# Performance work log

Measured on AMD Instinct MI355X. Metric: run time of the kernel, lower is better.

Reference implementation:

```python
import jax, jax.numpy as jnp
import numpy as np

B, C, N = 4, 128, 8192
CQK = C // 4  # query/key projection dim = out_channels // 4


def setup_inputs() -> dict:
    key = jax.random.key(0)
    ks = jax.random.split(key, 9)
    s_in = 1.0 / np.sqrt(C)
    return {
        "x": jax.random.normal(ks[0], (B, C, N), dtype=jnp.float32),
        "xyz": jax.random.normal(ks[1], (B, N, 3), dtype=jnp.float32),
        "Wq": jax.random.normal(ks[2], (CQK, C), dtype=jnp.float32) * s_in,
        "bq": jax.random.normal(ks[3], (CQK,), dtype=jnp.float32) * 0.01,
        "Wk": jax.random.normal(ks[4], (CQK, C), dtype=jnp.float32) * s_in,
        "bk": jax.random.normal(ks[5], (CQK,), dtype=jnp.float32) * 0.01,
        "Wv": jax.random.normal(ks[6], (C, C), dtype=jnp.float32) * s_in,
        "bv": jax.random.normal(ks[7], (C,), dtype=jnp.float32) * 0.01,
        "gamma": jax.random.normal(ks[8], (1,), dtype=jnp.float32) * 0.1,
    }


def reference(x, xyz, Wq, bq, Wk, bk, Wv, bv, gamma):
    # 1x1 Conv1d == per-point linear projection over channels
    q = jnp.einsum('oc,bcn->bon', Wq, x) + bq[None, :, None]   # (B, CQK, N)
    k = jnp.einsum('oc,bcn->bon', Wk, x) + bk[None, :, None]   # (B, CQK, N)
    v = jnp.einsum('oc,bcn->bon', Wv, x) + bv[None, :, None]   # (B, C, N)

    # energy[b, n, m] = <q[:, n], k[:, m]>
    energy = jnp.einsum('bcn,bcm->bnm', q, k)                  # (B, N, N)

    # positional correlation bias: normalize coords per point, cosine-sim matrix
    xyz_bcn = jnp.swapaxes(xyz, 1, 2)                          # (B, 3, N)
    xyz_norm = xyz_bcn / (jnp.linalg.norm(xyz_bcn, axis=1, keepdims=True) + 1e-8)
    pos_corr = jnp.einsum('bcn,bcm->bnm', xyz_norm, xyz_norm)  # (B, N, N)
    energy = energy + 0.1 * pos_corr

    attention = jax.nn.softmax(energy, axis=-1)                # rowwise over m

    # out[b, c, n] = sum_m v[b, c, m] * attention[b, n, m]
    out = jnp.einsum('bcm,bnm->bcn', v, attention)             # (B, C, N)
    return gamma * out + x
```

## Files before the change

### kernel.cpp

```cpp
#include <hip/hip_runtime.h>

#define NPTS 8192
#define NB 4
#define NCH 128
#define DQK 48
#define TK 64
#define SPLIT 4
#define KEYS_PER (NPTS / SPLIT)
#define ROUNDS (KEYS_PER / TK)
#define SH2 28.853901f
#define LOG2E 1.4426950408889634f

typedef unsigned short ushort_t;
typedef unsigned int uint_t;
typedef __attribute__((ext_vector_type(8))) short bf16x8;
typedef __attribute__((ext_vector_type(4))) float f32x4;
typedef __attribute__((ext_vector_type(16))) float f32x16;

static __device__ __forceinline__ ushort_t f2bf(float x) {
  union { float f; uint_t u; } v; v.f = x;
  uint_t r = v.u + 0x7fffu + ((v.u >> 16) & 1u);
  return (ushort_t)(r >> 16);
}
static __device__ __forceinline__ float bf2f(ushort_t u) {
  union { uint_t i; float f; } v; v.i = ((uint_t)u) << 16; return v.f;
}
static __device__ __forceinline__ int sig16(int n) {
  int g2 = (n >> 2) & 3;
  return (g2 == 1 || g2 == 2) ? (n ^ 0xC) : n;
}

typedef __attribute__((address_space(1))) void void_g;
typedef __attribute__((address_space(3))) void void_l;
static __device__ __forceinline__ void gload_lds16(const ushort_t* g, ushort_t* l) {
  __builtin_amdgcn_global_load_lds((void_g*)(ushort_t*)g, (void_l*)l, 16, 0, 0);
}

__global__ __launch_bounds__(512, 1)
void wprep_kernel(const float* __restrict__ Wq, const float* __restrict__ bq,
                  const float* __restrict__ Wk, const float* __restrict__ bk,
                  const float* __restrict__ Wv, const float* __restrict__ bv,
                  ushort_t* __restrict__ Wb, float* __restrict__ bias_pre) {
  const int z = blockIdx.x;
  const int ks = threadIdx.x >> 6;
  const int lane = threadIdx.x & 63;
  const int l31 = lane & 31, h = lane >> 5;
  const float* W = (z == 0) ? Wq : (z == 1) ? Wk : (Wv + (size_t)(z - 2) * 32 * 128);
  const float sc = (z == 0) ? LOG2E : 1.0f;
  const float* wr = W + l31 * 128 + ks * 16 + h * 8;
  union { ushort_t u[8]; bf16x8 v; } p;
#pragma unroll
  for (int j = 0; j < 8; ++j) p.u[j] = f2bf(wr[j] * sc);
  *(bf16x8*)(Wb + ((size_t)(z * 8 + ks) * 64 + lane) * 8) = p.v;
  if (z == 0 && threadIdx.x < 192) {
    int i = threadIdx.x;
    bias_pre[i] = (i < 32) ? bq[i] * LOG2E : (i < 64) ? bk[i - 32] : bv[i - 64];
  }
}

__global__ __launch_bounds__(256, 4)
void projm2_kernel(const float* __restrict__ x, const float* __restrict__ xyz,
                   const ushort_t* __restrict__ Wb,
                   const float* __restrict__ bias_pre,
                   ushort_t* __restrict__ Qb, ushort_t* __restrict__ Kb,
                   ushort_t* __restrict__ Vt) {
  const int tid = threadIdx.x;
  const int lane = tid & 63, wv = tid >> 6;
  const int l31 = lane & 31, h = lane >> 5;
  const int b = blockIdx.y;
  const int n = blockIdx.x * 128 + wv * 32 + l31;

  bf16x8 bfr[8];
  const float* xb = x + (size_t)b * NCH * NPTS + n;
#pragma unroll
  for (int ks = 0; ks < 8; ++ks) {
    const float* xc = xb + (size_t)(ks * 16 + h * 8) * NPTS;
    union { ushort_t u[8]; bf16x8 v; } p;
#pragma unroll
    for (int j = 0; j < 8; ++j) p.u[j] = f2bf(xc[(size_t)j * NPTS]);
    bfr[ks] = p.v;
  }

  float xa = xyz[((size_t)b * NPTS + n) * 3 + 0];
  float xc2 = xyz[((size_t)b * NPTS + n) * 3 + 1];
  float xd = xyz[((size_t)b * NPTS + n) * 3 + 2];
  float rinv = 1.0f / (sqrtf(xa * xa + xc2 * xc2 + xd * xd) + 1e-8f);

#pragma unroll 1
  for (int z = 0; z < 6; ++z) {
    f32x16 S;
#pragma unroll
    for (int r = 0; r < 16; ++r)
      S[r] = bias_pre[z * 32 + (r & 3) + 8 * (r >> 2) + 4 * h];
#pragma unroll
    for (int ks = 0; ks < 8; ++ks) {
      bf16x8 af = *(const bf16x8*)(Wb + ((size_t)(z * 8 + ks) * 64 + lane) * 8);
      S = __builtin_amdgcn_mfma_f32_32x32x16_bf16(af, bfr[ks], S, 0, 0, 0);
    }
    if (z <= 1) {
      float sc = (z == 0) ? LOG2E : 1.0f;
      ushort_t* dst = (z == 0 ? Qb : Kb) + ((size_t)b * NPTS + n) * DQK;
#pragma unroll
      for (int r = 0; r < 16; ++r)
        dst[(r & 3) + 8 * (r >> 2) + 4 * h] = f2bf(S[r]);
      float rn = 0.31622776601683794f * sc * rinv;
      union { ushort_t u[16]; bf16x8 v[2]; } t;
#pragma unroll
      for (int j = 0; j < 16; ++j) t.u[j] = 0;
      t.u[0] = f2bf(xa * rn); t.u[1] = f2bf(xc2 * rn); t.u[2] = f2bf(xd * rn);
      *(bf16x8*)(dst + 32) = t.v[0];
      *(bf16x8*)(dst + 40) = t.v[1];
    } else {
      const int np = (n & ~15) | sig16(n & 15);
      const int c0 = (z - 2) * 32;
#pragma unroll
      for (int r = 0; r < 16; ++r)
        Vt[((size_t)b * NCH + c0 + (r & 3) + 8 * (r >> 2) + 4 * h) * NPTS + np] =
            f2bf(S[r]);
    }
  }
}

__global__ __launch_bounds__(512, 2)
void attn32_kernel(const ushort_t* __restrict__ Qb, const ushort_t* __restrict__ Kb,
                   const ushort_t* __restrict__ Vt,
                   ushort_t* __restrict__ PACC, float* __restrict__ PL) {
  __shared__ __align__(16) ushort_t L[2][22][512];
  const int tid = threadIdx.x;
  const int lane = tid & 63, w = tid >> 6;
  const int l31 = lane & 31, h = lane >> 5;

  const int lin = blockIdx.x;
  const int bs = lin & 15;
  const int b = bs & 3, sseg = bs >> 2;
  const int qblk = lin >> 4;
  const int q0w = qblk * 512 + w * 64;
  const int m00 = sseg * KEYS_PER;

  bf16x8 qf[2][3];
#pragma unroll
  for (int g = 0; g < 2; ++g)
#pragma unroll
    for (int c = 0; c < 3; ++c)
      qf[g][c] = *(const bf16x8*)(Qb + ((size_t)b * NPTS + q0w + g * 32 + l31) * DQK +
                                  c * 16 + h * 8);

  const ushort_t* gp[3];
  int fid[3], adv[3];
  const int nf = (w < 6) ? 3 : 2;
  for (int i = 0; i < nf; ++i) {
    int fi = w + 8 * i;
    fid[i] = fi;
    if (fi < 6) {
      int kb = fi / 3, c = fi - kb * 3;
      gp[i] = Kb + ((size_t)b * NPTS + m00 + kb * 32 + l31) * DQK + c * 16 + h * 8;
      adv[i] = TK * DQK;
    } else {
      int vi = fi - 6, fch = vi >> 2, kk = vi & 3;
      gp[i] = Vt + ((size_t)b * NCH + fch * 32 + l31) * NPTS + m00 + kk * 16 + h * 8;
      adv[i] = TK;
    }
  }

  f32x16 O[2][4];
#pragma unroll
  for (int g = 0; g < 2; ++g)
#pragma unroll
    for (int f = 0; f < 4; ++f) O[g][f] = (f32x16)(0.f);
  float lsum0 = 0.f, lsum1 = 0.f;

  for (int i = 0; i < nf; ++i) gload_lds16(gp[i], &L[0][fid[i]][0]);

#pragma unroll 1
  for (int t = 0; t < ROUNDS; ++t) {
    __syncthreads();
    const int cur = t & 1;
    if (t + 1 < ROUNDS) {
      for (int i = 0; i < nf; ++i) {
        gp[i] += adv[i];
        gload_lds16(gp[i], &L[cur ^ 1][fid[i]][0]);
      }
    }

#pragma unroll
    for (int kb = 0; kb < 2; ++kb) {
      bf16x8 kf0 = *(const bf16x8*)(&L[cur][kb * 3 + 0][0] + lane * 8);
      bf16x8 kf1 = *(const bf16x8*)(&L[cur][kb * 3 + 1][0] + lane * 8);
      bf16x8 kf2 = *(const bf16x8*)(&L[cur][kb * 3 + 2][0] + lane * 8);

      uint_t pk[2][8];
#pragma unroll
      for (int g = 0; g < 2; ++g) {
        f32x16 S = __builtin_amdgcn_mfma_f32_32x32x16_bf16(kf0, qf[g][0], (f32x16)(0.f), 0, 0, 0);
        S = __builtin_amdgcn_mfma_f32_32x32x16_bf16(kf1, qf[g][1], S, 0, 0, 0);
        S = __builtin_amdgcn_mfma_f32_32x32x16_bf16(kf2, qf[g][2], S, 0, 0, 0);
        float p[16];
        float ts = 0.f;
#pragma unroll
        for (int r = 0; r < 16; ++r) {
          p[r] = __builtin_amdgcn_exp2f(S[r] - SH2);
          ts += p[r];
        }
        if (g == 0) lsum0 += ts; else lsum1 += ts;
#pragma unroll
        for (int i = 0; i < 8; ++i)
          pk[g][i] = __builtin_amdgcn_perm(__float_as_uint(p[2 * i + 1]),
                                           __float_as_uint(p[2 * i]), 0x07060302u);
      }

#pragma unroll
      for (int kkl = 0; kkl < 2; ++kkl) {
        bf16x8 A[2];
#pragma unroll
        for (int g = 0; g < 2; ++g) {
          union { uint_t u[4]; bf16x8 v; } au;
          au.u[0] = pk[g][4 * kkl + 0];
          au.u[1] = pk[g][4 * kkl + 1];
          au.u[2] = pk[g][4 * kkl + 2];
          au.u[3] = pk[g][4 * kkl + 3];
          A[g] = au.v;
        }
#pragma unroll
        for (int f = 0; f < 4; ++f) {
          bf16x8 vf = *(const bf16x8*)(&L[cur][6 + f * 4 + kb * 2 + kkl][0] + lane * 8);
          O[0][f] = __builtin_amdgcn_mfma_f32_32x32x16_bf16(A[0], vf, O[0][f], 0, 0, 0);
          O[1][f] = __builtin_amdgcn_mfma_f32_32x32x16_bf16(A[1], vf, O[1][f], 0, 0, 0);
        }
      }
    }
  }

  lsum0 += __shfl_xor(lsum0, 32);
  lsum1 += __shfl_xor(lsum1, 32);
  const size_t pbase = (((size_t)bs * 16 + qblk) * 8 + w) * 2;
#pragma unroll
  for (int g = 0; g < 2; ++g) {
#pragma unroll
    for (int f = 0; f < 4; ++f) {
      union { ushort_t u[16]; bf16x8 v[2]; } pu;
#pragma unroll
      for (int r = 0; r < 16; ++r) pu.u[r] = f2bf(O[g][f][r]);
      size_t idx = ((pbase + g) * 4 + f) * 1024 + (size_t)lane * 16;
      *(bf16x8*)(PACC + idx) = pu.v[0];
      *(bf16x8*)(PACC + idx + 8) = pu.v[1];
    }
    if (lane < 32)
      PL[(size_t)bs * NPTS + q0w + g * 32 + lane] = (g == 0) ? lsum0 : lsum1;
  }
}

#define MPITCH 268
__global__ __launch_bounds__(256, 4)
void merge4c_kernel(const ushort_t* __restrict__ PACC, const float* __restrict__ PL,
                    const float* __restrict__ x, const float* __restrict__ gamma,
                    float* __restrict__ out) {
  __shared__ float Linv[256];
  __shared__ float ldso[32 * MPITCH];
  const int tid = threadIdx.x;
  const int qblk2 = blockIdx.x, b = blockIdx.y, f = blockIdx.z;
  const int q0 = qblk2 * 256;

  float Ls = 0.f;
#pragma unroll
  for (int s = 0; s < 4; ++s)
    Ls += PL[(size_t)(s * 4 + b) * NPTS + q0 + tid];
  Linv[tid] = gamma[0] / Ls;
  __syncthreads();

  const int ww = tid >> 6, lane = tid & 63, l31 = lane & 31, h = lane >> 5;

#pragma unroll
  for (int g = 0; g < 2; ++g) {
    float acc[16];
#pragma unroll
    for (int r = 0; r < 16; ++r) acc[r] = 0.f;
#pragma unroll
    for (int s = 0; s < 4; ++s) {
      size_t idx = (((((size_t)(s * 4 + b) * 16 + (qblk2 >> 1)) * 8 +
                      (qblk2 & 1) * 4 + ww) * 2 + g) * 4 + f) * 1024 +
                   (size_t)lane * 16;
      bf16x8 a0 = *(const bf16x8*)(PACC + idx);
      bf16x8 a1 = *(const bf16x8*)(PACC + idx + 8);
#pragma unroll
      for (int r = 0; r < 8; ++r) {
        acc[r] += bf2f((ushort_t)a0[r]);
        acc[8 + r] += bf2f((ushort_t)a1[r]);
      }
    }
    const int qb = ww * 64 + g * 32 + 4 * h;
#pragma unroll
    for (int rr = 0; rr < 4; ++rr) {
      int q = qb + 8 * rr;
      f32x4 v;
#pragma unroll
      for (int i = 0; i < 4; ++i) v[i] = acc[rr * 4 + i] * Linv[q + i];
      *(f32x4*)&ldso[l31 * MPITCH + q] = v;
    }
  }
  __syncthreads();

  const float* xb = x + ((size_t)b * NCH + f * 32) * NPTS + q0;
  float* ob = out + ((size_t)b * NCH + f * 32) * NPTS + q0;
#pragma unroll
  for (int rr = 0; rr < 8; ++rr) {
    int ch = ww * 8 + rr;
    f32x4 v = *(const f32x4*)&ldso[ch * MPITCH + lane * 4];
    f32x4 xv = *(const f32x4*)(xb + (size_t)ch * NPTS + lane * 4);
    v += xv;
    *(f32x4*)(ob + (size_t)ch * NPTS + lane * 4) = v;
  }
}

extern "C" void kernel_launch(void* const* d_in, const int* in_sizes, int n_in,
                              void* d_out, int out_size, void* d_ws,
                              size_t ws_size, hipStream_t stream) {
  const float* x     = (const float*)d_in[0];
  const float* xyz   = (const float*)d_in[1];
  const float* Wq    = (const float*)d_in[2];
  const float* bq    = (const float*)d_in[3];
  const float* Wk    = (const float*)d_in[4];
  const float* bk    = (const float*)d_in[5];
  const float* Wv    = (const float*)d_in[6];
  const float* bv    = (const float*)d_in[7];
  const float* gamma = (const float*)d_in[8];
  float* out = (float*)d_out;

  const size_t BN = (size_t)NB * NPTS;
  ushort_t* Qb = (ushort_t*)d_ws;
  ushort_t* Kb = Qb + BN * DQK;
  ushort_t* Vt = Kb + BN * DQK;
  ushort_t* PACC = Vt + BN * NCH;
  float* PL = (float*)(PACC + (size_t)16 * 16 * 8 * 2 * 4 * 1024);
  ushort_t* Wb = (ushort_t*)(PL + 16 * BN / 2);
  float* bias_pre = (float*)(Wb + 6 * 8 * 64 * 8);

  wprep_kernel<<<6, 512, 0, stream>>>(Wq, bq, Wk, bk, Wv, bv, Wb, bias_pre);
  projm2_kernel<<<dim3(NPTS / 128, NB), 256, 0, stream>>>(
      x, xyz, Wb, bias_pre, Qb, Kb, Vt);
  attn32_kernel<<<256, 512, 0, stream>>>(Qb, Kb, Vt, PACC, PL);
  merge4c_kernel<<<dim3(32, NB, 4), 256, 0, stream>>>(PACC, PL, x, gamma, out);
  (void)in_sizes; (void)n_in; (void)out_size; (void)ws_size;
}
```

Before: 199.6 us.

## Halve per-wave query rows, fold softmax shift into QK dot, raise occupancy

Each wave now handles 32 query rows instead of 64, which halves the O accumulator registers and allows 4 blocks per CU with twice as many blocks launched. The constant softmax shift is folded into the QK matmul through an extra padded feature (-SH2 in Q, 1 in K), removing a subtraction per score. MFMA sections are wrapped in s_setprio and the load loops are fully unrolled. In exchange, each block reloads the K/V tiles for fewer queries, doubling K/V traffic per query, and the bf16-rounded shift adds small numeric error.

Measured after the change: 190.6 us. -4.5%, faster.

```diff
diff --git a/kernel.cpp b/kernel.cpp
--- a/kernel.cpp
+++ b/kernel.cpp
@@ -108,6 +108,7 @@
 #pragma unroll
       for (int j = 0; j < 16; ++j) t.u[j] = 0;
       t.u[0] = f2bf(xa * rn); t.u[1] = f2bf(xc2 * rn); t.u[2] = f2bf(xd * rn);
+      t.u[3] = (z == 0) ? f2bf(-SH2) : f2bf(1.0f);
       *(bf16x8*)(dst + 32) = t.v[0];
       *(bf16x8*)(dst + 40) = t.v[1];
     } else {
@@ -121,7 +122,7 @@
   }
 }
 
-__global__ __launch_bounds__(512, 2)
+__global__ __launch_bounds__(512, 4)
 void attn32_kernel(const ushort_t* __restrict__ Qb, const ushort_t* __restrict__ Kb,
                    const ushort_t* __restrict__ Vt,
                    ushort_t* __restrict__ PACC, float* __restrict__ PL) {
@@ -134,52 +135,53 @@
   const int bs = lin & 15;
   const int b = bs & 3, sseg = bs >> 2;
   const int qblk = lin >> 4;
-  const int q0w = qblk * 512 + w * 64;
+  const int q0w = qblk * 256 + w * 32;
   const int m00 = sseg * KEYS_PER;
 
-  bf16x8 qf[2][3];
-#pragma unroll
-  for (int g = 0; g < 2; ++g)
-#pragma unroll
-    for (int c = 0; c < 3; ++c)
-      qf[g][c] = *(const bf16x8*)(Qb + ((size_t)b * NPTS + q0w + g * 32 + l31) * DQK +
-                                  c * 16 + h * 8);
+  bf16x8 qf[3];
+#pragma unroll
+  for (int c = 0; c < 3; ++c)
+    qf[c] = *(const bf16x8*)(Qb + ((size_t)b * NPTS + q0w + l31) * DQK +
+                             c * 16 + h * 8);
 
   const ushort_t* gp[3];
   int fid[3], adv[3];
   const int nf = (w < 6) ? 3 : 2;
-  for (int i = 0; i < nf; ++i) {
+#pragma unroll
+  for (int i = 0; i < 3; ++i) {
     int fi = w + 8 * i;
     fid[i] = fi;
     if (fi < 6) {
       int kb = fi / 3, c = fi - kb * 3;
       gp[i] = Kb + ((size_t)b * NPTS + m00 + kb * 32 + l31) * DQK + c * 16 + h * 8;
       adv[i] = TK * DQK;
-    } else {
+    } else if (fi < 22) {
       int vi = fi - 6, fch = vi >> 2, kk = vi & 3;
       gp[i] = Vt + ((size_t)b * NCH + fch * 32 + l31) * NPTS + m00 + kk * 16 + h * 8;
       adv[i] = TK;
     }
   }
 
-  f32x16 O[2][4];
-#pragma unroll
-  for (int g = 0; g < 2; ++g)
-#pragma unroll
-    for (int f = 0; f < 4; ++f) O[g][f] = (f32x16)(0.f);
-  float lsum0 = 0.f, lsum1 = 0.f;
-
-  for (int i = 0; i < nf; ++i) gload_lds16(gp[i], &L[0][fid[i]][0]);
+  f32x16 O[4];
+#pragma unroll
+  for (int f = 0; f < 4; ++f) O[f] = (f32x16)(0.f);
+  float ls0 = 0.f, ls1 = 0.f;
+
+#pragma unroll
+  for (int i = 0; i < 3; ++i)
+    if (i < nf) gload_lds16(gp[i], &L[0][fid[i]][0]);
 
 #pragma unroll 1
   for (int t = 0; t < ROUNDS; ++t) {
     __syncthreads();
     const int cur = t & 1;
     if (t + 1 < ROUNDS) {
-      for (int i = 0; i < nf; ++i) {
-        gp[i] += adv[i];
-        gload_lds16(gp[i], &L[cur ^ 1][fid[i]][0]);
-      }
+#pragma unroll
+      for (int i = 0; i < 3; ++i)
+        if (i < nf) {
+          gp[i] += adv[i];
+          gload_lds16(gp[i], &L[cur ^ 1][fid[i]][0]);
+        }
     }
 
 #pragma unroll
@@ -188,65 +190,56 @@
       bf16x8 kf1 = *(const bf16x8*)(&L[cur][kb * 3 + 1][0] + lane * 8);
       bf16x8 kf2 = *(const bf16x8*)(&L[cur][kb * 3 + 2][0] + lane * 8);
 
-      uint_t pk[2][8];
-#pragma unroll
-      for (int g = 0; g < 2; ++g) {
-        f32x16 S = __builtin_amdgcn_mfma_f32_32x32x16_bf16(kf0, qf[g][0], (f32x16)(0.f), 0, 0, 0);
-        S = __builtin_amdgcn_mfma_f32_32x32x16_bf16(kf1, qf[g][1], S, 0, 0, 0);
-        S = __builtin_amdgcn_mfma_f32_32x32x16_bf16(kf2, qf[g][2], S, 0, 0, 0);
-        float p[16];
-        float ts = 0.f;
-#pragma unroll
-        for (int r = 0; r < 16; ++r) {
-          p[r] = __builtin_amdgcn_exp2f(S[r] - SH2);
-          ts += p[r];
-        }
-        if (g == 0) lsum0 += ts; else lsum1 += ts;
-#pragma unroll
-        for (int i = 0; i < 8; ++i)
-          pk[g][i] = __builtin_amdgcn_perm(__float_as_uint(p[2 * i + 1]),
-                                           __float_as_uint(p[2 * i]), 0x07060302u);
+      __builtin_amdgcn_s_setprio(1);
+      f32x16 S = __builtin_amdgcn_mfma_f32_32x32x16_bf16(kf0, qf[0],
+                                                         (f32x16)(0.f), 0, 0, 0);
+      S = __builtin_amdgcn_mfma_f32_32x32x16_bf16(kf1, qf[1], S, 0, 0, 0);
+      S = __builtin_amdgcn_mfma_f32_32x32x16_bf16(kf2, qf[2], S, 0, 0, 0);
+      __builtin_amdgcn_s_setprio(0);
+
+      uint_t pk[8];
+#pragma unroll
+      for (int i = 0; i < 8; ++i) {
+        float p0 = __builtin_amdgcn_exp2f(S[2 * i]);
+        float p1 = __builtin_amdgcn_exp2f(S[2 * i + 1]);
+        ls0 += p0;
+        ls1 += p1;
+        pk[i] = __builtin_amdgcn_perm(__float_as_uint(p1), __float_as_uint(p0),
+                                      0x07060302u);
       }
 
 #pragma unroll
       for (int kkl = 0; kkl < 2; ++kkl) {
-        bf16x8 A[2];
-#pragma unroll
-        for (int g = 0; g < 2; ++g) {
-          union { uint_t u[4]; bf16x8 v; } au;
-          au.u[0] = pk[g][4 * kkl + 0];
-          au.u[1] = pk[g][4 * kkl + 1];
-          au.u[2] = pk[g][4 * kkl + 2];
-          au.u[3] = pk[g][4 * kkl + 3];
-          A[g] = au.v;
-        }
+        union { uint_t u[4]; bf16x8 v; } au;
+        au.u[0] = pk[4 * kkl + 0];
+        au.u[1] = pk[4 * kkl + 1];
+        au.u[2] = pk[4 * kkl + 2];
+        au.u[3] = pk[4 * kkl + 3];
+        bf16x8 A = au.v;
+        __builtin_amdgcn_s_setprio(1);
 #pragma unroll
         for (int f = 0; f < 4; ++f) {
           bf16x8 vf = *(const bf16x8*)(&L[cur][6 + f * 4 + kb * 2 + kkl][0] + lane * 8);
-          O[0][f] = __builtin_amdgcn_mfma_f32_32x32x16_bf16(A[0], vf, O[0][f], 0, 0, 0);
-          O[1][f] = __builtin_amdgcn_mfma_f32_32x32x16_bf16(A[1], vf, O[1][f], 0, 0, 0);
+          O[f] = __builtin_amdgcn_mfma_f32_32x32x16_bf16(A, vf, O[f], 0, 0, 0);
         }
+        __builtin_amdgcn_s_setprio(0);
       }
     }
   }
 
-  lsum0 += __shfl_xor(lsum0, 32);
-  lsum1 += __shfl_xor(lsum1, 32);
-  const size_t pbase = (((size_t)bs * 16 + qblk) * 8 + w) * 2;
-#pragma unroll
-  for (int g = 0; g < 2; ++g) {
-#pragma unroll
-    for (int f = 0; f < 4; ++f) {
-      union { ushort_t u[16]; bf16x8 v[2]; } pu;
-#pragma unroll
-      for (int r = 0; r < 16; ++r) pu.u[r] = f2bf(O[g][f][r]);
-      size_t idx = ((pbase + g) * 4 + f) * 1024 + (size_t)lane * 16;
-      *(bf16x8*)(PACC + idx) = pu.v[0];
-      *(bf16x8*)(PACC + idx + 8) = pu.v[1];
-    }
-    if (lane < 32)
-      PL[(size_t)bs * NPTS + q0w + g * 32 + lane] = (g == 0) ? lsum0 : lsum1;
-  }
+  float lsum = ls0 + ls1;
+  lsum += __shfl_xor(lsum, 32);
+  const size_t pbase = (size_t)(bs * 16 + (qblk >> 1)) * 16 + (qblk & 1) * 8 + w;
+#pragma unroll
+  for (int f = 0; f < 4; ++f) {
+    union { ushort_t u[16]; bf16x8 v[2]; } pu;
+#pragma unroll
+    for (int r = 0; r < 16; ++r) pu.u[r] = f2bf(O[f][r]);
+    size_t idx = (pbase * 4 + f) * 1024 + (size_t)lane * 16;
+    *(bf16x8*)(PACC + idx) = pu.v[0];
+    *(bf16x8*)(PACC + idx + 8) = pu.v[1];
+  }
+  if (lane < 32) PL[(size_t)bs * NPTS + q0w + lane] = lsum;
 }
 
 #define MPITCH 268
@@ -337,7 +330,7 @@
   wprep_kernel<<<6, 512, 0, stream>>>(Wq, bq, Wk, bk, Wv, bv, Wb, bias_pre);
   projm2_kernel<<<dim3(NPTS / 128, NB), 256, 0, stream>>>(
       x, xyz, Wb, bias_pre, Qb, Kb, Vt);
-  attn32_kernel<<<256, 512, 0, stream>>>(Qb, Kb, Vt, PACC, PL);
+  attn32_kernel<<<512, 512, 0, stream>>>(Qb, Kb, Vt, PACC, PL);
   merge4c_kernel<<<dim3(32, NB, 4), 256, 0, stream>>>(PACC, PL, x, gamma, out);
   (void)in_sizes; (void)n_in; (void)out_size; (void)ws_size;
 }
```

## Fold softmax shift into Q/K padding, halve attention blocks, add MFMA priority hints

Applied to the files above, without the earlier changes.

Adds a constant column to the padded Q/K vectors (-SH2 in Q, 1 in K) so the fixed exponent shift comes out of the MFMA dot product, which removes a subtract per score. The attention kernel moves from 512-thread to 256-thread blocks over twice as many blocks, so each wave now issues more global-to-LDS loads for the shared K/V tile. It also wraps the MFMA groups in s_setprio and interleaves exp2 with bf16 packing. The goal is better scheduling and occupancy, at the cost of each block reusing a loaded K/V tile across half as many queries.

Measured after the change: 240.0 us. +20.2%, slower.

```diff
diff --git a/kernel.cpp b/kernel.cpp
--- a/kernel.cpp
+++ b/kernel.cpp
@@ -108,6 +108,7 @@
 #pragma unroll
       for (int j = 0; j < 16; ++j) t.u[j] = 0;
       t.u[0] = f2bf(xa * rn); t.u[1] = f2bf(xc2 * rn); t.u[2] = f2bf(xd * rn);
+      t.u[3] = (z == 0) ? f2bf(-SH2) : f2bf(1.0f);
       *(bf16x8*)(dst + 32) = t.v[0];
       *(bf16x8*)(dst + 40) = t.v[1];
     } else {
@@ -121,7 +122,7 @@
   }
 }
 
-__global__ __launch_bounds__(512, 2)
+__global__ __launch_bounds__(256, 2)
 void attn32_kernel(const ushort_t* __restrict__ Qb, const ushort_t* __restrict__ Kb,
                    const ushort_t* __restrict__ Vt,
                    ushort_t* __restrict__ PACC, float* __restrict__ PL) {
@@ -134,7 +135,7 @@
   const int bs = lin & 15;
   const int b = bs & 3, sseg = bs >> 2;
   const int qblk = lin >> 4;
-  const int q0w = qblk * 512 + w * 64;
+  const int q0w = qblk * 256 + w * 64;
   const int m00 = sseg * KEYS_PER;
 
   bf16x8 qf[2][3];
@@ -145,17 +146,18 @@
       qf[g][c] = *(const bf16x8*)(Qb + ((size_t)b * NPTS + q0w + g * 32 + l31) * DQK +
                                   c * 16 + h * 8);
 
-  const ushort_t* gp[3];
-  int fid[3], adv[3];
-  const int nf = (w < 6) ? 3 : 2;
-  for (int i = 0; i < nf; ++i) {
-    int fi = w + 8 * i;
+  const ushort_t* gp[6];
+  int fid[6], adv[6];
+  const int nf = (w < 2) ? 6 : 5;
+#pragma unroll
+  for (int i = 0; i < 6; ++i) {
+    int fi = w + 4 * i;
     fid[i] = fi;
     if (fi < 6) {
       int kb = fi / 3, c = fi - kb * 3;
       gp[i] = Kb + ((size_t)b * NPTS + m00 + kb * 32 + l31) * DQK + c * 16 + h * 8;
       adv[i] = TK * DQK;
-    } else {
+    } else if (fi < 22) {
       int vi = fi - 6, fch = vi >> 2, kk = vi & 3;
       gp[i] = Vt + ((size_t)b * NCH + fch * 32 + l31) * NPTS + m00 + kk * 16 + h * 8;
       adv[i] = TK;
@@ -167,19 +169,23 @@
   for (int g = 0; g < 2; ++g)
 #pragma unroll
     for (int f = 0; f < 4; ++f) O[g][f] = (f32x16)(0.f);
-  float lsum0 = 0.f, lsum1 = 0.f;
-
-  for (int i = 0; i < nf; ++i) gload_lds16(gp[i], &L[0][fid[i]][0]);
+  float ls0 = 0.f, ls1 = 0.f;
+
+#pragma unroll
+  for (int i = 0; i < 6; ++i)
+    if (i < nf) gload_lds16(gp[i], &L[0][fid[i]][0]);
 
 #pragma unroll 1
   for (int t = 0; t < ROUNDS; ++t) {
     __syncthreads();
     const int cur = t & 1;
     if (t + 1 < ROUNDS) {
-      for (int i = 0; i < nf; ++i) {
-        gp[i] += adv[i];
-        gload_lds16(gp[i], &L[cur ^ 1][fid[i]][0]);
-      }
+#pragma unroll
+      for (int i = 0; i < 6; ++i)
+        if (i < nf) {
+          gp[i] += adv[i];
+          gload_lds16(gp[i], &L[cur ^ 1][fid[i]][0]);
+        }
     }
 
 #pragma unroll
@@ -191,21 +197,23 @@
       uint_t pk[2][8];
 #pragma unroll
       for (int g = 0; g < 2; ++g) {
-        f32x16 S = __builtin_amdgcn_mfma_f32_32x32x16_bf16(kf0, qf[g][0], (f32x16)(0.f), 0, 0, 0);
+        __builtin_amdgcn_s_setprio(1);
+        f32x16 S = __builtin_amdgcn_mfma_f32_32x32x16_bf16(kf0, qf[g][0],
+                                                           (f32x16)(0.f), 0, 0, 0);
         S = __builtin_amdgcn_mfma_f32_32x32x16_bf16(kf1, qf[g][1], S, 0, 0, 0);
         S = __builtin_amdgcn_mfma_f32_32x32x16_bf16(kf2, qf[g][2], S, 0, 0, 0);
-        float p[16];
+        __builtin_amdgcn_s_setprio(0);
         float ts = 0.f;
 #pragma unroll
-        for (int r = 0; r < 16; ++r) {
-          p[r] = __builtin_amdgcn_exp2f(S[r] - SH2);
-          ts += p[r];
+        for (int i = 0; i < 8; ++i) {
+          float p0 = __builtin_amdgcn_exp2f(S[2 * i]);
+          float p1 = __builtin_amdgcn_exp2f(S[2 * i + 1]);
+          ts += p0;
+          ts += p1;
+          pk[g][i] = __builtin_amdgcn_perm(__float_as_uint(p1), __float_as_uint(p0),
+                                           0x07060302u);
         }
-        if (g == 0) lsum0 += ts; else lsum1 += ts;
-#pragma unroll
-        for (int i = 0; i < 8; ++i)
-          pk[g][i] = __builtin_amdgcn_perm(__float_as_uint(p[2 * i + 1]),
-                                           __float_as_uint(p[2 * i]), 0x07060302u);
+        if (g == 0) ls0 += ts; else ls1 += ts;
       }
 
 #pragma unroll
@@ -220,19 +228,21 @@
           au.u[3] = pk[g][4 * kkl + 3];
           A[g] = au.v;
         }
+        __builtin_amdgcn_s_setprio(1);
 #pragma unroll
         for (int f = 0; f < 4; ++f) {
           bf16x8 vf = *(const bf16x8*)(&L[cur][6 + f * 4 + kb * 2 + kkl][0] + lane * 8);
           O[0][f] = __builtin_amdgcn_mfma_f32_32x32x16_bf16(A[0], vf, O[0][f], 0, 0, 0);
           O[1][f] = __builtin_amdgcn_mfma_f32_32x32x16_bf16(A[1], vf, O[1][f], 0, 0, 0);
         }
+        __builtin_amdgcn_s_setprio(0);
       }
     }
   }
 
-  lsum0 += __shfl_xor(lsum0, 32);
-  lsum1 += __shfl_xor(lsum1, 32);
-  const size_t pbase = (((size_t)bs * 16 + qblk) * 8 + w) * 2;
+  ls0 += __shfl_xor(ls0, 32);
+  ls1 += __shfl_xor(ls1, 32);
+  const size_t pb0 = (size_t)(bs * 16 + (qblk >> 1)) * 16 + (qblk & 1) * 8 + w * 2;
 #pragma unroll
   for (int g = 0; g < 2; ++g) {
 #pragma unroll
@@ -240,12 +250,12 @@
       union { ushort_t u[16]; bf16x8 v[2]; } pu;
 #pragma unroll
       for (int r = 0; r < 16; ++r) pu.u[r] = f2bf(O[g][f][r]);
-      size_t idx = ((pbase + g) * 4 + f) * 1024 + (size_t)lane * 16;
+      size_t idx = ((pb0 + g) * 4 + f) * 1024 + (size_t)lane * 16;
       *(bf16x8*)(PACC + idx) = pu.v[0];
       *(bf16x8*)(PACC + idx + 8) = pu.v[1];
     }
     if (lane < 32)
-      PL[(size_t)bs * NPTS + q0w + g * 32 + lane] = (g == 0) ? lsum0 : lsum1;
+      PL[(size_t)bs * NPTS + q0w + g * 32 + lane] = (g == 0) ? ls0 : ls1;
   }
 }
 
@@ -337,7 +347,7 @@
   wprep_kernel<<<6, 512, 0, stream>>>(Wq, bq, Wk, bk, Wv, bv, Wb, bias_pre);
   projm2_kernel<<<dim3(NPTS / 128, NB), 256, 0, stream>>>(
       x, xyz, Wb, bias_pre, Qb, Kb, Vt);
-  attn32_kernel<<<256, 512, 0, stream>>>(Qb, Kb, Vt, PACC, PL);
+  attn32_kernel<<<512, 256, 0, stream>>>(Qb, Kb, Vt, PACC, PL);
   merge4c_kernel<<<dim3(32, NB, 4), 256, 0, stream>>>(PACC, PL, x, gamma, out);
   (void)in_sizes; (void)n_in; (void)out_size; (void)ws_size;
 }
```
